# Performance work log

Hardware: AMD Instinct MI355X
Metric: run time of the kernel (lower is better)

## Reference

```python
import jax, jax.numpy as jnp
import numpy as np

B, T, D, H, L = 64, 512, 512, 512, 2


def setup_inputs() -> dict:
    key = jax.random.key(0)
    ks = jax.random.split(key, 9)
    std = 1.0 / np.sqrt(H)
    u = lambda k, shape: jax.random.uniform(k, shape, jnp.float32, -std, std)
    return {
        "x": jax.random.normal(ks[0], (B, T, D), jnp.float32),
        "Wx0": u(ks[1], (4 * H, D)), "bx0": u(ks[2], (4 * H,)),
        "Wh0": u(ks[3], (4 * H, H)), "bh0": u(ks[4], (4 * H,)),
        "Wx1": u(ks[5], (4 * H, H)), "bx1": u(ks[6], (4 * H,)),
        "Wh1": u(ks[7], (4 * H, H)), "bh1": u(ks[8], (4 * H,)),
    }


def _lstm_layer(x_seq, Wx, bx, Wh, bh):
    # x_seq: [T, B, D_in] -> hidden sequence [T, B, H]
    h0 = jnp.zeros((x_seq.shape[1], Wh.shape[1]), x_seq.dtype)
    c0 = jnp.zeros_like(h0)
    # precompute input projections for all steps (one big GEMM)
    xg = jnp.einsum('tbd,gd->tbg', x_seq, Wx) + bx + bh  # [T, B, 4H]

    def step(carry, xg_t):
        h, c = carry
        gates = xg_t + h @ Wh.T
        f, i, g, o = jnp.split(gates, 4, axis=1)
        f = jax.nn.sigmoid(f)
        i = jax.nn.sigmoid(i)
        g = jnp.tanh(g)
        o = jax.nn.sigmoid(o)
        c = f * c + i * g
        h = o * jnp.tanh(c)
        return (h, c), h

    (_, _), hs = jax.lax.scan(step, (h0, c0), xg)
    return hs


def reference(x, Wx0, bx0, Wh0, bh0, Wx1, bx1, Wh1, bh1):
    xs = jnp.transpose(x, (1, 0, 2))  # [T, B, D]
    h1 = _lstm_layer(xs, Wx0, bx0, Wh0, bh0)   # [T, B, H]
    h2 = _lstm_layer(h1, Wx1, bx1, Wh1, bh1)   # [T, B, H]
    return h2[-1]  # last hidden state of top layer: [B, H]
```

## Files before the change

kernel.cpp:

```cpp
#include <hip/hip_runtime.h>
#include <hip/hip_bf16.h>
#include <stdint.h>

#define T_STEPS 512
#define BATCH   64
#define HID     512
#define DIN     512
#define G4      2048
#define HBLK_T  32768
#define SENT8   0xFFFFFFFFFFFFFFFFull

typedef __attribute__((ext_vector_type(8))) short bf16x8;
typedef __attribute__((ext_vector_type(4))) float f32x4;
typedef __attribute__((ext_vector_type(4))) unsigned short us4;
typedef unsigned long long ull;

static __device__ __forceinline__ unsigned short f2bf(float f) {
  union { float f; unsigned u; } v; v.f = f;
  unsigned r = v.u + 0x7FFFu + ((v.u >> 16) & 1u);
  return (unsigned short)(r >> 16);
}
static __device__ __forceinline__ float bf2f(unsigned short s) {
  union { unsigned u; float f; } v; v.u = ((unsigned)s) << 16;
  return v.f;
}
static __device__ __forceinline__ float sigf(float x) { return 1.f / (1.f + __expf(-x)); }
static __device__ __forceinline__ float tanh_fast(float x) {
  x = fminf(15.f, fmaxf(-15.f, x));
  float e = __expf(2.f * x);
  return (e - 1.f) / (e + 1.f);
}

__global__ void cvt_f32_bf16(const float* __restrict__ src, unsigned short* __restrict__ dst, long n) {
  long i = (long)blockIdx.x * blockDim.x + threadIdx.x;
  long st = (long)gridDim.x * blockDim.x;
  for (; i < n; i += st) dst[i] = f2bf(src[i]);
}

__global__ __launch_bounds__(256) void proj_kernel(
    const float* __restrict__ x,
    const unsigned short* __restrict__ Wb,
    const float* __restrict__ ba,
    const float* __restrict__ bb,
    unsigned short* __restrict__ xg) {
  __shared__ unsigned short xt[64 * 512];
  const int t   = blockIdx.x;
  const int tid = threadIdx.x;

  for (int i = 0; i < 16; ++i) {
    const int c    = i * 256 + tid;
    const int b    = c >> 6;
    const int col8 = c & 63;
    const float* src = x + ((long)b * T_STEPS + t) * DIN + col8 * 8;
    f32x4 v0 = *(const f32x4*)(src);
    f32x4 v1 = *(const f32x4*)(src + 4);
    union { unsigned short s[8]; bf16x8 v; } u;
    #pragma unroll
    for (int e = 0; e < 4; ++e) { u.s[e] = f2bf(v0[e]); u.s[4 + e] = f2bf(v1[e]); }
    const int byteoff = b * 1024 + ((col8 * 16) ^ ((b & 7) << 4));
    *(bf16x8*)((char*)xt + byteoff) = u.v;
  }
  __syncthreads();

  const int wv   = tid >> 6;
  const int lane = tid & 63;
  const int n16  = lane & 15;
  const int q    = lane >> 4;
  const int kof  = q * 8;

  for (int gt = 0; gt < 32; ++gt) {
    const int g0 = wv * 512 + gt * 16;
    const unsigned short* ap = Wb + (long)(g0 + n16) * DIN + kof;
    f32x4 acc[4];
    #pragma unroll
    for (int nb = 0; nb < 4; ++nb) acc[nb] = (f32x4){0.f, 0.f, 0.f, 0.f};
    #pragma unroll
    for (int kk = 0; kk < 16; ++kk) {
      bf16x8 a = *(const bf16x8*)(ap + kk * 32);
      const int colb = (kof + kk * 32) * 2;
      #pragma unroll
      for (int nb = 0; nb < 4; ++nb) {
        const int row = nb * 16 + n16;
        bf16x8 bv = *(const bf16x8*)((const char*)xt + row * 1024 + (colb ^ ((row & 7) << 4)));
        acc[nb] = __builtin_amdgcn_mfma_f32_16x16x32_bf16(a, bv, acc[nb], 0, 0, 0);
      }
    }
    const int m0 = q * 4;
    #pragma unroll
    for (int r = 0; r < 4; ++r) {
      const int g = g0 + m0 + r;
      const float bv = ba[g] + bb[g];
      long base = ((long)t * G4 + g) * BATCH + n16;
      xg[base +  0] = f2bf(acc[0][r] + bv);
      xg[base + 16] = f2bf(acc[1][r] + bv);
      xg[base + 32] = f2bf(acc[2][r] + bv);
      xg[base + 48] = f2bf(acc[3][r] + bv);
    }
  }
}

__global__ __launch_bounds__(128, 1) void fused_rec(
    const float* __restrict__ Wh0,
    const float* __restrict__ Wx1,
    const float* __restrict__ Wh1,
    const float* __restrict__ bx1, const float* __restrict__ bh1,
    const unsigned short* __restrict__ xg0,
    unsigned short* __restrict__ hseq1,
    unsigned short* __restrict__ hseq2,
    float* __restrict__ out,
    int T) {
  __shared__ unsigned short whl0[32 * 512];
  __shared__ unsigned short whl1[32 * 1024];
  __shared__ __align__(16) unsigned short hsc[2][128];

  const int bid  = blockIdx.x;
  const int gq   = bid & 3;
  const int j    = bid >> 2;
  const int wv   = threadIdx.x >> 6;
  const int lane = threadIdx.x & 63;
  const int hidbase = j * 8;
  const int n16  = lane & 15;
  const int q    = lane >> 4;
  const int kof  = q * 8;
  const int bloc = q * 4;
  const int rr0 = n16, rr1 = 16 + n16;
  const int grow0 = (rr0 >> 3) * HID + hidbase + (rr0 & 7);
  const int grow1 = (rr1 >> 3) * HID + hidbase + (rr1 & 7);
  const int rdbase = gq * 128 + n16 * 8;
  const int myblk  = (j * 4 + gq) * 128;

  auto cv8 = [](const float* s) -> bf16x8 {
    f32x4 a = *(const f32x4*)s, b = *(const f32x4*)(s + 4);
    union { unsigned short u[8]; bf16x8 v; } w;
    #pragma unroll
    for (int e = 0; e < 4; ++e) { w.u[e] = f2bf(a[e]); w.u[4 + e] = f2bf(b[e]); }
    return w.v;
  };
  if (wv == 0) {
    for (int r = 0; r < 32; ++r) {
      const long grow = (long)(r >> 3) * HID + hidbase + (r & 7);
      bf16x8 v = cv8(Wh0 + grow * HID + lane * 8);
      *(bf16x8*)((char*)whl0 + r * 1024 + ((lane * 16) ^ ((r & 7) << 4))) = v;
    }
  } else {
    for (int r = 0; r < 32; ++r) {
      const long grow = (long)(r >> 3) * HID + hidbase + (r & 7);
      bf16x8 va = cv8(Wx1 + grow * HID + lane * 8);
      bf16x8 vb = cv8(Wh1 + grow * HID + lane * 8);
      const int rb = r * 2048;
      *(bf16x8*)((char*)whl1 + rb + ((lane * 16) ^ ((r & 7) << 4))) = va;
      *(bf16x8*)((char*)whl1 + rb + ((1024 + lane * 16) ^ ((r & 7) << 4))) = vb;
    }
  }
  __syncthreads();

  if (wv == 0) {
    float c4[4] = {0.f, 0.f, 0.f, 0.f};
    for (int t = 0; t < T; ++t) {
      us4 xv0 = *(const us4*)(xg0 + ((long)t * G4 + grow0) * BATCH + gq * 16 + bloc);
      us4 xv1 = *(const us4*)(xg0 + ((long)t * G4 + grow1) * BATCH + gq * 16 + bloc);

      f32x4 acc0 = {0.f,0.f,0.f,0.f}, acc1 = {0.f,0.f,0.f,0.f};
      if (t > 0) {
        const ull* hp = (const ull*)(hseq1 + (long)(t - 1) * HBLK_T + rdbase);
        ull lo[16], hi[16];
        int bad;
        do {
          bad = 0;
          #pragma unroll
          for (int kk = 0; kk < 16; ++kk) {
            const int boff = (kk * 4 + q) * 128;
            lo[kk] = __hip_atomic_load(hp + boff,     __ATOMIC_RELAXED, __HIP_MEMORY_SCOPE_AGENT);
            hi[kk] = __hip_atomic_load(hp + boff + 1, __ATOMIC_RELAXED, __HIP_MEMORY_SCOPE_AGENT);
          }
          #pragma unroll
          for (int kk = 0; kk < 16; ++kk)
            bad |= (lo[kk] == SENT8) | (hi[kk] == SENT8);
        } while (__any(bad));
        #pragma unroll
        for (int kk = 0; kk < 16; ++kk) {
          union { ull qq[2]; bf16x8 v; } u; u.qq[0] = lo[kk]; u.qq[1] = hi[kk];
          const int colb = (kof + kk * 32) * 2;
          bf16x8 b0 = *(const bf16x8*)((const char*)whl0 + rr0 * 1024 + (colb ^ ((rr0 & 7) << 4)));
          bf16x8 b1 = *(const bf16x8*)((const char*)whl0 + rr1 * 1024 + (colb ^ ((rr1 & 7) << 4)));
          acc0 = __builtin_amdgcn_mfma_f32_16x16x32_bf16(u.v, b0, acc0, 0, 0, 0);
          acc1 = __builtin_amdgcn_mfma_f32_16x16x32_bf16(u.v, b1, acc1, 0, 0, 0);
        }
      }
      #pragma unroll
      for (int r = 0; r < 4; ++r) { acc0[r] += bf2f(xv0[r]); acc1[r] += bf2f(xv1[r]); }

      f32x4 o0, o1;
      #pragma unroll
      for (int r = 0; r < 4; ++r) {
        o0[r] = __shfl_xor(acc0[r], 8, 64);
        o1[r] = __shfl_xor(acc1[r], 8, 64);
      }
      if (n16 < 8) {
        #pragma unroll
        for (int r = 0; r < 4; ++r) {
          const float fg = sigf(acc0[r]);
          const float ig = sigf(o0[r]);
          const float gg = tanh_fast(acc1[r]);
          const float og = sigf(o1[r]);
          const float cn = fg * c4[r] + ig * gg;
          c4[r] = cn;
          const float h = og * tanh_fast(cn);
          *(unsigned short*)((char*)hsc[0] + (bloc + r) * 16 + n16 * 2) = f2bf(h);
        }
      }
      asm volatile("s_waitcnt lgkmcnt(0)" ::: "memory");
      if (lane < 32) {
        ull v8 = *(const ull*)((const char*)hsc[0] + lane * 8);
        ull* dst = (ull*)(hseq1 + (long)t * HBLK_T + myblk) + lane;
        __hip_atomic_store(dst, v8, __ATOMIC_RELAXED, __HIP_MEMORY_SCOPE_AGENT);
      }
    }
  } else {
    float c4[4] = {0.f, 0.f, 0.f, 0.f};
    const float b0v = bx1[grow0] + bh1[grow0];
    const float b1v = bx1[grow1] + bh1[grow1];
    for (int t = 0; t < T; ++t) {
      ull la[16], ha[16], lb[16], hb[16];
      const ull* pa = (const ull*)(hseq1 + (long)t * HBLK_T + rdbase);
      const ull* pb = (const ull*)(hseq2 + (long)(t - 1) * HBLK_T + rdbase);
      #pragma unroll
      for (int kk = 0; kk < 16; ++kk) {
        const int boff = (kk * 4 + q) * 128;
        la[kk] = __hip_atomic_load(pa + boff,     __ATOMIC_RELAXED, __HIP_MEMORY_SCOPE_AGENT);
        ha[kk] = __hip_atomic_load(pa + boff + 1, __ATOMIC_RELAXED, __HIP_MEMORY_SCOPE_AGENT);
      }
      if (t > 0) {
        #pragma unroll
        for (int kk = 0; kk < 16; ++kk) {
          const int boff = (kk * 4 + q) * 128;
          lb[kk] = __hip_atomic_load(pb + boff,     __ATOMIC_RELAXED, __HIP_MEMORY_SCOPE_AGENT);
          hb[kk] = __hip_atomic_load(pb + boff + 1, __ATOMIC_RELAXED, __HIP_MEMORY_SCOPE_AGENT);
        }
      }
      for (;;) {
        int bad = 0;
        #pragma unroll
        for (int kk = 0; kk < 16; ++kk) bad |= (la[kk] == SENT8) | (ha[kk] == SENT8);
        if (!__any(bad)) break;
        #pragma unroll
        for (int kk = 0; kk < 16; ++kk) {
          const int boff = (kk * 4 + q) * 128;
          la[kk] = __hip_atomic_load(pa + boff,     __ATOMIC_RELAXED, __HIP_MEMORY_SCOPE_AGENT);
          ha[kk] = __hip_atomic_load(pa + boff + 1, __ATOMIC_RELAXED, __HIP_MEMORY_SCOPE_AGENT);
        }
      }
      f32x4 acc0 = {0.f,0.f,0.f,0.f}, acc1 = {0.f,0.f,0.f,0.f};
      #pragma unroll
      for (int kk = 0; kk < 16; ++kk) {
        union { ull qq[2]; bf16x8 v; } u; u.qq[0] = la[kk]; u.qq[1] = ha[kk];
        const int colb = (kof + kk * 32) * 2;
        bf16x8 b0 = *(const bf16x8*)((const char*)whl1 + rr0 * 2048 + (colb ^ ((rr0 & 7) << 4)));
        bf16x8 b1 = *(const bf16x8*)((const char*)whl1 + rr1 * 2048 + (colb ^ ((rr1 & 7) << 4)));
        acc0 = __builtin_amdgcn_mfma_f32_16x16x32_bf16(u.v, b0, acc0, 0, 0, 0);
        acc1 = __builtin_amdgcn_mfma_f32_16x16x32_bf16(u.v, b1, acc1, 0, 0, 0);
      }
      if (t > 0) {
        for (;;) {
          int bad = 0;
          #pragma unroll
          for (int kk = 0; kk < 16; ++kk) bad |= (lb[kk] == SENT8) | (hb[kk] == SENT8);
          if (!__any(bad)) break;
          #pragma unroll
          for (int kk = 0; kk < 16; ++kk) {
            const int boff = (kk * 4 + q) * 128;
            lb[kk] = __hip_atomic_load(pb + boff,     __ATOMIC_RELAXED, __HIP_MEMORY_SCOPE_AGENT);
            hb[kk] = __hip_atomic_load(pb + boff + 1, __ATOMIC_RELAXED, __HIP_MEMORY_SCOPE_AGENT);
          }
        }
        #pragma unroll
        for (int kk = 0; kk < 16; ++kk) {
          union { ull qq[2]; bf16x8 v; } u; u.qq[0] = lb[kk]; u.qq[1] = hb[kk];
          const int colb = 1024 + (kof + kk * 32) * 2;
          bf16x8 b0 = *(const bf16x8*)((const char*)whl1 + rr0 * 2048 + (colb ^ ((rr0 & 7) << 4)));
          bf16x8 b1 = *(const bf16x8*)((const char*)whl1 + rr1 * 2048 + (colb ^ ((rr1 & 7) << 4)));
          acc0 = __builtin_amdgcn_mfma_f32_16x16x32_bf16(u.v, b0, acc0, 0, 0, 0);
          acc1 = __builtin_amdgcn_mfma_f32_16x16x32_bf16(u.v, b1, acc1, 0, 0, 0);
        }
      }
      #pragma unroll
      for (int r = 0; r < 4; ++r) { acc0[r] += b0v; acc1[r] += b1v; }

      f32x4 o0, o1;
      #pragma unroll
      for (int r = 0; r < 4; ++r) {
        o0[r] = __shfl_xor(acc0[r], 8, 64);
        o1[r] = __shfl_xor(acc1[r], 8, 64);
      }
      if (n16 < 8) {
        const int hid = hidbase + n16;
        #pragma unroll
        for (int r = 0; r < 4; ++r) {
          const float fg = sigf(acc0[r]);
          const float ig = sigf(o0[r]);
          const float gg = tanh_fast(acc1[r]);
          const float og = sigf(o1[r]);
          const float cn = fg * c4[r] + ig * gg;
          c4[r] = cn;
          const float h = og * tanh_fast(cn);
          *(unsigned short*)((char*)hsc[1] + (bloc + r) * 16 + n16 * 2) = f2bf(h);
          if (t == T - 1) out[(long)(gq * 16 + bloc + r) * HID + hid] = h;
        }
      }
      asm volatile("s_waitcnt lgkmcnt(0)" ::: "memory");
      if (lane < 32) {
        ull v8 = *(const ull*)((const char*)hsc[1] + lane * 8);
        ull* dst = (ull*)(hseq2 + (long)t * HBLK_T + myblk) + lane;
        __hip_atomic_store(dst, v8, __ATOMIC_RELAXED, __HIP_MEMORY_SCOPE_AGENT);
      }
    }
  }
}

extern "C" void kernel_launch(void* const* d_in, const int* in_sizes, int n_in,
                              void* d_out, int out_size, void* d_ws, size_t ws_size,
                              hipStream_t stream) {
  const float* x   = (const float*)d_in[0];
  const float* Wx0 = (const float*)d_in[1];
  const float* bx0 = (const float*)d_in[2];
  const float* Wh0 = (const float*)d_in[3];
  const float* bh0 = (const float*)d_in[4];
  const float* Wx1 = (const float*)d_in[5];
  const float* bx1 = (const float*)d_in[6];
  const float* Wh1 = (const float*)d_in[7];
  const float* bh1 = (const float*)d_in[8];

  char* ws = (char*)d_ws;
  size_t off = 0;
  auto alloc = [&](size_t bytes) -> char* {
    char* p = ws + off; off += (bytes + 255) & ~(size_t)255; return p;
  };
  unsigned short* xg    = (unsigned short*)alloc((size_t)T_STEPS * G4 * BATCH * 2);
  unsigned short* hseq1 = (unsigned short*)alloc((size_t)T_STEPS * HBLK_T * 2);
  unsigned short* hseq2 = (unsigned short*)alloc((size_t)T_STEPS * HBLK_T * 2);
  unsigned short* Wx0b  = (unsigned short*)alloc((size_t)G4 * DIN * 2);

  hipMemsetAsync(hseq1, 0xFF, (size_t)T_STEPS * HBLK_T * 2, stream);
  hipMemsetAsync(hseq2, 0xFF, (size_t)T_STEPS * HBLK_T * 2, stream);

  cvt_f32_bf16<<<1024, 256, 0, stream>>>(Wx0, Wx0b, (long)G4 * DIN);

  proj_kernel<<<T_STEPS, 256, 0, stream>>>(x, Wx0b, bx0, bh0, xg);
  fused_rec<<<256, 128, 0, stream>>>(Wh0, Wx1, Wh1, bx1, bh1,
                                     xg, hseq1, hseq2, (float*)d_out, T_STEPS);
}
```

Measured before the change: 2.504 ms.

## Forward layer-0 hidden states to layer-1 wave via shared-memory ring buffer

The layer-0 wave already polls h1[t-1] from global memory for its own recurrence. It now copies those values into a double-buffered LDS ring and signals through workgroup-scope flags. The layer-1 wave reads its input from LDS instead of issuing its own polling global atomic loads for h1[t]. This removes redundant global/L2 traffic and spin polling by the second wave, but it couples the two waves through intra-block spin waits. That coupling can stall layer 0 when layer 1 falls behind, and the ring buffer uses 32KB more LDS.

```diff
diff --git a/kernel.cpp b/kernel.cpp
--- a/kernel.cpp
+++ b/kernel.cpp
@@ -111,7 +111,9 @@
     int T) {
   __shared__ unsigned short whl0[32 * 512];
   __shared__ unsigned short whl1[32 * 1024];
+  __shared__ __align__(16) unsigned short ring[2 * 64 * 128];
   __shared__ __align__(16) unsigned short hsc[2][128];
+  __shared__ int l0_wr, l1_rd;
 
   const int bid  = blockIdx.x;
   const int gq   = bid & 3;
@@ -128,6 +130,9 @@
   const int grow1 = (rr1 >> 3) * HID + hidbase + (rr1 & 7);
   const int rdbase = gq * 128 + n16 * 8;
   const int myblk  = (j * 4 + gq) * 128;
+  const int rsw    = (lane & 7) << 4;
+
+  if (threadIdx.x == 0) { l0_wr = 0; l1_rd = 0; }
 
   auto cv8 = [](const float* s) -> bf16x8 {
     f32x4 a = *(const f32x4*)s, b = *(const f32x4*)(s + 4);
@@ -160,10 +165,10 @@
       us4 xv0 = *(const us4*)(xg0 + ((long)t * G4 + grow0) * BATCH + gq * 16 + bloc);
       us4 xv1 = *(const us4*)(xg0 + ((long)t * G4 + grow1) * BATCH + gq * 16 + bloc);
 
+      ull lo[16], hi[16];
       f32x4 acc0 = {0.f,0.f,0.f,0.f}, acc1 = {0.f,0.f,0.f,0.f};
       if (t > 0) {
         const ull* hp = (const ull*)(hseq1 + (long)(t - 1) * HBLK_T + rdbase);
-        ull lo[16], hi[16];
         int bad;
         do {
           bad = 0;
@@ -215,21 +220,57 @@
         ull* dst = (ull*)(hseq1 + (long)t * HBLK_T + myblk) + lane;
         __hip_atomic_store(dst, v8, __ATOMIC_RELAXED, __HIP_MEMORY_SCOPE_AGENT);
       }
+      if (t > 0) {
+        while (__hip_atomic_load(&l1_rd, __ATOMIC_RELAXED, __HIP_MEMORY_SCOPE_WORKGROUP) < t - 2) {}
+        __builtin_amdgcn_sched_barrier(0);
+        char* slot = (char*)ring + ((t - 1) & 1) * 16384 + lane * 256;
+        #pragma unroll
+        for (int kk = 0; kk < 16; ++kk) {
+          union { ull qq[2]; bf16x8 v; } u; u.qq[0] = lo[kk]; u.qq[1] = hi[kk];
+          *(bf16x8*)(slot + ((kk * 16) ^ rsw)) = u.v;
+        }
+        asm volatile("s_waitcnt lgkmcnt(0)" ::: "memory");
+        __builtin_amdgcn_sched_barrier(0);
+        if (lane == 0)
+          __hip_atomic_store(&l0_wr, t, __ATOMIC_RELAXED, __HIP_MEMORY_SCOPE_WORKGROUP);
+      }
+    }
+    {
+      const ull* hp = (const ull*)(hseq1 + (long)(T - 1) * HBLK_T + rdbase);
+      ull lo[16], hi[16];
+      int bad;
+      do {
+        bad = 0;
+        #pragma unroll
+        for (int kk = 0; kk < 16; ++kk) {
+          const int boff = (kk * 4 + q) * 128;
+          lo[kk] = __hip_atomic_load(hp + boff,     __ATOMIC_RELAXED, __HIP_MEMORY_SCOPE_AGENT);
+          hi[kk] = __hip_atomic_load(hp + boff + 1, __ATOMIC_RELAXED, __HIP_MEMORY_SCOPE_AGENT);
+        }
+        #pragma unroll
+        for (int kk = 0; kk < 16; ++kk)
+          bad |= (lo[kk] == SENT8) | (hi[kk] == SENT8);
+      } while (__any(bad));
+      while (__hip_atomic_load(&l1_rd, __ATOMIC_RELAXED, __HIP_MEMORY_SCOPE_WORKGROUP) < T - 2) {}
+      __builtin_amdgcn_sched_barrier(0);
+      char* slot = (char*)ring + ((T - 1) & 1) * 16384 + lane * 256;
+      #pragma unroll
+      for (int kk = 0; kk < 16; ++kk) {
+        union { ull qq[2]; bf16x8 v; } u; u.qq[0] = lo[kk]; u.qq[1] = hi[kk];
+        *(bf16x8*)(slot + ((kk * 16) ^ rsw)) = u.v;
+      }
+      asm volatile("s_waitcnt lgkmcnt(0)" ::: "memory");
+      __builtin_amdgcn_sched_barrier(0);
+      if (lane == 0)
+        __hip_atomic_store(&l0_wr, T, __ATOMIC_RELAXED, __HIP_MEMORY_SCOPE_WORKGROUP);
     }
   } else {
     float c4[4] = {0.f, 0.f, 0.f, 0.f};
     const float b0v = bx1[grow0] + bh1[grow0];
     const float b1v = bx1[grow1] + bh1[grow1];
     for (int t = 0; t < T; ++t) {
-      ull la[16], ha[16], lb[16], hb[16];
-      const ull* pa = (const ull*)(hseq1 + (long)t * HBLK_T + rdbase);
+      ull lb[16], hb[16];
       const ull* pb = (const ull*)(hseq2 + (long)(t - 1) * HBLK_T + rdbase);
-      #pragma unroll
-      for (int kk = 0; kk < 16; ++kk) {
-        const int boff = (kk * 4 + q) * 128;
-        la[kk] = __hip_atomic_load(pa + boff,     __ATOMIC_RELAXED, __HIP_MEMORY_SCOPE_AGENT);
-        ha[kk] = __hip_atomic_load(pa + boff + 1, __ATOMIC_RELAXED, __HIP_MEMORY_SCOPE_AGENT);
-      }
       if (t > 0) {
         #pragma unroll
         for (int kk = 0; kk < 16; ++kk) {
@@ -238,27 +279,25 @@
           hb[kk] = __hip_atomic_load(pb + boff + 1, __ATOMIC_RELAXED, __HIP_MEMORY_SCOPE_AGENT);
         }
       }
-      for (;;) {
-        int bad = 0;
-        #pragma unroll
-        for (int kk = 0; kk < 16; ++kk) bad |= (la[kk] == SENT8) | (ha[kk] == SENT8);
-        if (!__any(bad)) break;
-        #pragma unroll
-        for (int kk = 0; kk < 16; ++kk) {
-          const int boff = (kk * 4 + q) * 128;
-          la[kk] = __hip_atomic_load(pa + boff,     __ATOMIC_RELAXED, __HIP_MEMORY_SCOPE_AGENT);
-          ha[kk] = __hip_atomic_load(pa + boff + 1, __ATOMIC_RELAXED, __HIP_MEMORY_SCOPE_AGENT);
-        }
-      }
+      while (__hip_atomic_load(&l0_wr, __ATOMIC_RELAXED, __HIP_MEMORY_SCOPE_WORKGROUP) < t + 1) {}
+      __builtin_amdgcn_sched_barrier(0);
+      bf16x8 ra[16];
+      const char* slot = (const char*)ring + (t & 1) * 16384 + lane * 256;
+      #pragma unroll
+      for (int kk = 0; kk < 16; ++kk)
+        ra[kk] = *(const bf16x8*)(slot + ((kk * 16) ^ rsw));
+      asm volatile("s_waitcnt lgkmcnt(0)" ::: "memory");
+      __builtin_amdgcn_sched_barrier(0);
+      if (lane == 0)
+        __hip_atomic_store(&l1_rd, t + 1, __ATOMIC_RELAXED, __HIP_MEMORY_SCOPE_WORKGROUP);
       f32x4 acc0 = {0.f,0.f,0.f,0.f}, acc1 = {0.f,0.f,0.f,0.f};
       #pragma unroll
       for (int kk = 0; kk < 16; ++kk) {
-        union { ull qq[2]; bf16x8 v; } u; u.qq[0] = la[kk]; u.qq[1] = ha[kk];
         const int colb = (kof + kk * 32) * 2;
         bf16x8 b0 = *(const bf16x8*)((const char*)whl1 + rr0 * 2048 + (colb ^ ((rr0 & 7) << 4)));
         bf16x8 b1 = *(const bf16x8*)((const char*)whl1 + rr1 * 2048 + (colb ^ ((rr1 & 7) << 4)));
-        acc0 = __builtin_amdgcn_mfma_f32_16x16x32_bf16(u.v, b0, acc0, 0, 0, 0);
-        acc1 = __builtin_amdgcn_mfma_f32_16x16x32_bf16(u.v, b1, acc1, 0, 0, 0);
+        acc0 = __builtin_amdgcn_mfma_f32_16x16x32_bf16(ra[kk], b0, acc0, 0, 0, 0);
+        acc1 = __builtin_amdgcn_mfma_f32_16x16x32_bf16(ra[kk], b1, acc1, 0, 0, 0);
       }
       if (t > 0) {
         for (;;) {
```

Result: faster. 2.087 ms (-16.7%).
